# Kernel optimization log

Hardware: AMD Instinct MI355X
Metric: run time of the kernel (lower is better)

Reference implementation:

```python
import jax, jax.numpy as jnp
import numpy as np

V = 196608      # HEALPix nside=128 vertices
DEG = 9         # nnz per row (8 neighbors + self)
C = 64          # in_channels == out_channels
K = 8           # Chebyshev kernel_size
B = 1
EPS = 1e-5


def setup_inputs() -> dict:
    key = jax.random.key(0)
    ks = jax.random.split(key, 8)
    nnz = V * DEG
    x = jax.random.normal(ks[0], (B, V, C), dtype=jnp.float32)
    lap_rows = jnp.repeat(jnp.arange(V, dtype=jnp.int64), DEG)
    lap_cols = jax.random.randint(ks[1], (nnz,), 0, V, dtype=jnp.int64)
    lap_vals = jax.random.normal(ks[2], (nnz,), dtype=jnp.float32) * 0.1
    gamma = jnp.ones((C,), dtype=jnp.float32)
    beta = jnp.zeros((C,), dtype=jnp.float32)
    # Chebyshev weight [K, Fin, Fout], kaiming-like scale
    weight = jax.random.normal(ks[3], (K, C, C), dtype=jnp.float32) * (1.0 / np.sqrt(C * K))
    bias = jnp.zeros((C,), dtype=jnp.float32)
    return {"x": x, "lap_rows": lap_rows, "lap_cols": lap_cols, "lap_vals": lap_vals,
            "gamma": gamma, "beta": beta, "weight": weight, "bias": bias}


def _mish(h):
    return h * jnp.tanh(jax.nn.softplus(h))


def reference(x, lap_rows, lap_cols, lap_vals, gamma, beta, weight, bias):
    Bb, Vv, Cc = x.shape
    Kk = weight.shape[0]
    # BatchNorm1d (training-mode batch stats) over (B, V) per channel
    mean = jnp.mean(x, axis=(0, 1))
    var = jnp.var(x, axis=(0, 1))
    h = (x - mean) * jax.lax.rsqrt(var + EPS) * gamma + beta
    # Mish activation
    h = _mish(h)
    # Chebyshev spectral conv: x_k = 2*L@x_{k-1} - x_{k-2}
    def lap_mm(y):  # y: [V, M] sparse L @ y via gather + segment-sum scatter
        return jax.ops.segment_sum(lap_vals[:, None] * y[lap_cols], lap_rows,
                                   num_segments=Vv)
    x0 = jnp.transpose(h, (1, 0, 2)).reshape(Vv, Bb * Cc)  # [V, B*Fin]
    xs = [x0]
    if Kk > 1:
        xs.append(lap_mm(x0))
    for _ in range(2, Kk):
        xs.append(2.0 * lap_mm(xs[-1]) - xs[-2])
    Xk = jnp.stack(xs, axis=0).reshape(Kk, Vv, Bb, Cc)  # [K, V, B, Fin]
    out = jnp.einsum('kvbi,kio->bvo', Xk, weight) + bias  # [B, V, Fout]
    return out
```

## Files before the change

### kernel.cpp

```cpp
#include <hip/hip_runtime.h>
#include <math.h>

#define NV 196608
#define NDEG 9
#define NC 64
#define NK 8
#define TILE 64
#define NBLK (NV / TILE)
#define LDA 72
static constexpr float EPS = 1e-5f;

typedef __attribute__((ext_vector_type(8))) short bf16x8;
typedef __attribute__((ext_vector_type(4))) short bf16x4;
typedef __attribute__((ext_vector_type(4))) float f32x4;

__device__ __forceinline__ short f2bf(float f) {
    unsigned u = __float_as_uint(f);
    unsigned r = (u + 0x7fffu + ((u >> 16) & 1u)) >> 16;
    return (short)r;
}
__device__ __forceinline__ float bf2f(short h) {
    return __uint_as_float(((unsigned)(unsigned short)h) << 16);
}

__device__ __forceinline__ float mish_f(float h) {
    float t = __expf(fminf(h, 20.f));
    float p = 1.f + t;
    float p2 = p * p;
    return h * ((p2 - 1.f) / (p2 + 1.f));
}

__global__ void __launch_bounds__(256) stats_kernel(const float* __restrict__ x,
                                                    float* __restrict__ stats) {
    const float4* x4 = (const float4*)x;
    int t = blockIdx.x * 256 + threadIdx.x;
    int stride = gridDim.x * 256;
    float4 s = {0.f, 0.f, 0.f, 0.f}, ss = {0.f, 0.f, 0.f, 0.f};
    for (int i = t; i < NV * (NC / 4); i += stride) {
        float4 v = x4[i];
        s.x += v.x; s.y += v.y; s.z += v.z; s.w += v.w;
        ss.x += v.x * v.x; ss.y += v.y * v.y; ss.z += v.z * v.z; ss.w += v.w * v.w;
    }
    __shared__ float4 ls[256], lss[256];
    ls[threadIdx.x] = s;
    lss[threadIdx.x] = ss;
    __syncthreads();
    if (threadIdx.x < 64) {
        int ch = threadIdx.x;
        int g = ch >> 2, comp = ch & 3;
        float a = 0.f, b = 0.f;
        #pragma unroll
        for (int k = 0; k < 16; ++k) {
            float4 v1 = ls[k * 16 + g];
            float4 v2 = lss[k * 16 + g];
            a += (comp == 0) ? v1.x : (comp == 1) ? v1.y : (comp == 2) ? v1.z : v1.w;
            b += (comp == 0) ? v2.x : (comp == 1) ? v2.y : (comp == 2) ? v2.z : v2.w;
        }
        atomicAdd(&stats[ch], a);
        atomicAdd(&stats[64 + ch], b);
    }
}

__global__ void __launch_bounds__(256) wconv_kernel(const float* __restrict__ w,
                                                    unsigned short* __restrict__ Wb) {
    int idx = blockIdx.x * 256 + threadIdx.x;
    int i = idx & 63, o = (idx >> 6) & 63, k = idx >> 12;
    Wb[idx] = (unsigned short)f2bf(w[k * 4096 + i * 64 + o]);
}

__global__ void __launch_bounds__(256) bn_mish_k0(
    const float* __restrict__ x, const float* __restrict__ stats,
    const float* __restrict__ gamma, const float* __restrict__ beta,
    unsigned short* __restrict__ dst) {
    int lane = threadIdx.x & 63;
    int wave = threadIdx.x >> 6;
    int c4 = lane & 15, rg = lane >> 4;
    int tile0 = blockIdx.x * TILE;

    float4 sc, sh;
    {
        float4 su = ((const float4*)stats)[c4];
        float4 sq = ((const float4*)stats)[16 + c4];
        float4 g4 = ((const float4*)gamma)[c4];
        float4 b4 = ((const float4*)beta)[c4];
        #define BNC(comp) { float mu = su.comp * (1.f / NV);                     \
                            float va = sq.comp * (1.f / NV) - mu * mu;           \
                            float rs = rsqrtf(va + EPS);                         \
                            sc.comp = g4.comp * rs;                              \
                            sh.comp = b4.comp - mu * sc.comp; }
        BNC(x) BNC(y) BNC(z) BNC(w)
        #undef BNC
    }

    const float4* x4 = (const float4*)x;
    #pragma unroll
    for (int it = 0; it < 4; ++it) {
        int v = tile0 + wave * 16 + it * 4 + rg;
        float4 h = x4[v * 16 + c4];
        float4 m;
        m.x = mish_f(h.x * sc.x + sh.x);
        m.y = mish_f(h.y * sc.y + sh.y);
        m.z = mish_f(h.z * sc.z + sh.z);
        m.w = mish_f(h.w * sc.w + sh.w);
        bf16x4 xb = { f2bf(m.x), f2bf(m.y), f2bf(m.z), f2bf(m.w) };
        *(bf16x4*)(dst + (size_t)v * NC + 4 * c4) = xb;
    }
}

template <bool FIRST>
__global__ void __launch_bounds__(256) cheb_step(
    const int* __restrict__ cols, const float* __restrict__ vals,
    const unsigned short* __restrict__ src, const unsigned short* __restrict__ prev,
    unsigned short* __restrict__ dst) {
    int lane = threadIdx.x & 63;
    int wave = threadIdx.x >> 6;
    int c8 = lane & 7, rg = lane >> 3;
    int tile0 = blockIdx.x * TILE;

    #pragma unroll
    for (int it = 0; it < 2; ++it) {
        int v = tile0 + wave * 16 + it * 8 + rg;
        const int* cp = cols + v * NDEG;
        const float* vp = vals + v * NDEG;
        float s[8] = {0.f, 0.f, 0.f, 0.f, 0.f, 0.f, 0.f, 0.f};
        #pragma unroll
        for (int j = 0; j < NDEG; ++j) {
            int cj = cp[j];
            float aj = vp[j];
            bf16x8 g = *(const bf16x8*)(src + (size_t)cj * NC + c8 * 8);
            #pragma unroll
            for (int q = 0; q < 8; ++q) s[q] += aj * bf2f(g[q]);
        }
        bf16x8 xb;
        if (FIRST) {
            #pragma unroll
            for (int q = 0; q < 8; ++q) xb[q] = f2bf(s[q]);
        } else {
            bf16x8 p = *(const bf16x8*)(prev + (size_t)v * NC + c8 * 8);
            #pragma unroll
            for (int q = 0; q < 8; ++q) xb[q] = f2bf(2.f * s[q] - bf2f(p[q]));
        }
        *(bf16x8*)(dst + (size_t)v * NC + c8 * 8) = xb;
    }
}

__global__ void __launch_bounds__(256) gemm_bases(
    const unsigned short* __restrict__ basis, const unsigned short* __restrict__ Wb,
    const float* __restrict__ bias, float* __restrict__ out,
    int kb, int kc, int S, int first) {
    __shared__ short At[TILE * LDA];
    __shared__ short Wt[NC * LDA];
    int tid = threadIdx.x;
    int lane = tid & 63, wave = tid >> 6;
    int m16 = lane & 15, qq = lane >> 4;
    int tile0 = blockIdx.x * TILE;

    f32x4 acc[4];
    #pragma unroll
    for (int nt = 0; nt < 4; ++nt) acc[nt] = (f32x4){0.f, 0.f, 0.f, 0.f};

    #pragma unroll 1
    for (int j = 0; j < kc; ++j) {
        int k = kb + j;
        const unsigned short* bs = basis + (size_t)(k % S) * NV * NC + (size_t)tile0 * NC;
        const unsigned short* wsrc = Wb + (size_t)k * NC * NC;
        __syncthreads();
        #pragma unroll
        for (int h = 0; h < 2; ++h) {
            int ci = tid + h * 256;
            int r = ci >> 3, c = ci & 7;
            *(bf16x8*)&At[r * LDA + c * 8] = *(const bf16x8*)(bs + ci * 8);
            *(bf16x8*)&Wt[r * LDA + c * 8] = *(const bf16x8*)(wsrc + ci * 8);
        }
        __syncthreads();
        bf16x8 a0 = *(const bf16x8*)&At[(wave * 16 + m16) * LDA + qq * 8];
        bf16x8 a1 = *(const bf16x8*)&At[(wave * 16 + m16) * LDA + 32 + qq * 8];
        #pragma unroll
        for (int nt = 0; nt < 4; ++nt) {
            bf16x8 b0 = *(const bf16x8*)&Wt[(nt * 16 + m16) * LDA + qq * 8];
            bf16x8 b1 = *(const bf16x8*)&Wt[(nt * 16 + m16) * LDA + 32 + qq * 8];
            acc[nt] = __builtin_amdgcn_mfma_f32_16x16x32_bf16(a0, b0, acc[nt], 0, 0, 0);
            acc[nt] = __builtin_amdgcn_mfma_f32_16x16x32_bf16(a1, b1, acc[nt], 0, 0, 0);
        }
    }

    #pragma unroll
    for (int nt = 0; nt < 4; ++nt) {
        float bcol = bias[nt * 16 + m16];
        #pragma unroll
        for (int r = 0; r < 4; ++r) {
            int vout = tile0 + wave * 16 + qq * 4 + r;
            float* po = out + (size_t)vout * NC + nt * 16 + m16;
            *po = first ? (acc[nt][r] + bcol) : (*po + acc[nt][r]);
        }
    }
}

extern "C" void kernel_launch(void* const* d_in, const int* in_sizes, int n_in,
                              void* d_out, int out_size, void* d_ws, size_t ws_size,
                              hipStream_t stream) {
    const float* x      = (const float*)d_in[0];
    const int*   cols   = (const int*)  d_in[2];
    const float* vals   = (const float*)d_in[3];
    const float* gamma  = (const float*)d_in[4];
    const float* beta   = (const float*)d_in[5];
    const float* weight = (const float*)d_in[6];
    const float* bias   = (const float*)d_in[7];
    float* out = (float*)d_out;

    char* wsb = (char*)d_ws;
    float*          stats = (float*)wsb;
    unsigned short* Wb    = (unsigned short*)(wsb + 1024);
    unsigned short* basis = (unsigned short*)(wsb + 131072);
    const size_t SLOT = (size_t)NV * NC;

    int S = (int)((ws_size - 131072) / (SLOT * sizeof(unsigned short)));
    if (S > NK) S = NK;
    if (S < 3) S = 3;

    hipMemsetAsync(stats, 0, 1024, stream);
    wconv_kernel<<<128, 256, 0, stream>>>(weight, Wb);
    stats_kernel<<<1024, 256, 0, stream>>>(x, stats);
    bn_mish_k0<<<NBLK, 256, 0, stream>>>(x, stats, gamma, beta, basis);

    int kb = 0, gsize = S, first = 1;
    while (kb < NK) {
        int kc = (gsize < NK - kb) ? gsize : (NK - kb);
        for (int k = (kb == 0 ? 1 : kb); k < kb + kc; ++k) {
            const unsigned short* src = basis + (size_t)((k - 1) % S) * SLOT;
            unsigned short*       dst = basis + (size_t)(k % S) * SLOT;
            if (k == 1) {
                cheb_step<true><<<NBLK, 256, 0, stream>>>(cols, vals, src, src, dst);
            } else {
                const unsigned short* prev = basis + (size_t)((k - 2) % S) * SLOT;
                cheb_step<false><<<NBLK, 256, 0, stream>>>(cols, vals, src, prev, dst);
            }
        }
        gemm_bases<<<NBLK, 256, 0, stream>>>(basis, Wb, bias, out, kb, kc, S, first);
        first = 0;
        kb += kc;
        gsize = S - 2;
    }
}
```

Before: 458.0 us.

## Merge stats/weight kernels, batch gathers, drop LDS staging in GEMM, split GEMM

Folds the weight bf16 conversion into the stats kernel as extra blocks, so one launch is saved. In cheb_step, the column indices and values are now loaded as vectors, all nine neighbour gathers are issued before accumulating, and the prev/dst accesses use nontemporal hints. gemm_bases now reads A and W fragments straight from global memory instead of staging them through LDS with barriers. When the workspace holds all eight bases, the first GEMM runs over k=0..3 right after basis 3 is built, and a second GEMM covers k=4..7. The risks are more registers from the batched gathers and uncoalesced, repeated W reads without LDS.

Result: slower. 557.8 us (+21.8%).

```diff
diff --git a/kernel.cpp b/kernel.cpp
--- a/kernel.cpp
+++ b/kernel.cpp
@@ -7,12 +7,14 @@
 #define NK 8
 #define TILE 64
 #define NBLK (NV / TILE)
-#define LDA 72
+#define SLOT ((size_t)NV * NC)
 static constexpr float EPS = 1e-5f;
 
 typedef __attribute__((ext_vector_type(8))) short bf16x8;
 typedef __attribute__((ext_vector_type(4))) short bf16x4;
 typedef __attribute__((ext_vector_type(4))) float f32x4;
+typedef int   i32x4u __attribute__((ext_vector_type(4), aligned(4)));
+typedef float f32x4u __attribute__((ext_vector_type(4), aligned(4)));
 
 __device__ __forceinline__ short f2bf(float f) {
     unsigned u = __float_as_uint(f);
@@ -30,11 +32,18 @@
     return h * ((p2 - 1.f) / (p2 + 1.f));
 }
 
-__global__ void __launch_bounds__(256) stats_kernel(const float* __restrict__ x,
-                                                    float* __restrict__ stats) {
+__global__ void __launch_bounds__(256) stats_wconv_kernel(
+    const float* __restrict__ x, float* __restrict__ stats,
+    const float* __restrict__ w, unsigned short* __restrict__ Wb) {
+    if (blockIdx.x >= 1024) {
+        int idx = (blockIdx.x - 1024) * 256 + threadIdx.x;
+        int i = idx & 63, o = (idx >> 6) & 63, k = idx >> 12;
+        Wb[idx] = (unsigned short)f2bf(w[k * 4096 + i * 64 + o]);
+        return;
+    }
     const float4* x4 = (const float4*)x;
     int t = blockIdx.x * 256 + threadIdx.x;
-    int stride = gridDim.x * 256;
+    int stride = 1024 * 256;
     float4 s = {0.f, 0.f, 0.f, 0.f}, ss = {0.f, 0.f, 0.f, 0.f};
     for (int i = t; i < NV * (NC / 4); i += stride) {
         float4 v = x4[i];
@@ -59,13 +68,6 @@
         atomicAdd(&stats[ch], a);
         atomicAdd(&stats[64 + ch], b);
     }
-}
-
-__global__ void __launch_bounds__(256) wconv_kernel(const float* __restrict__ w,
-                                                    unsigned short* __restrict__ Wb) {
-    int idx = blockIdx.x * 256 + threadIdx.x;
-    int i = idx & 63, o = (idx >> 6) & 63, k = idx >> 12;
-    Wb[idx] = (unsigned short)f2bf(w[k * 4096 + i * 64 + o]);
 }
 
 __global__ void __launch_bounds__(256) bn_mish_k0(
@@ -122,25 +124,40 @@
         int v = tile0 + wave * 16 + it * 8 + rg;
         const int* cp = cols + v * NDEG;
         const float* vp = vals + v * NDEG;
+        i32x4u c03 = __builtin_nontemporal_load((const i32x4u*)cp);
+        i32x4u c47 = __builtin_nontemporal_load((const i32x4u*)(cp + 4));
+        int    cl8 = __builtin_nontemporal_load(cp + 8);
+        f32x4u a03 = __builtin_nontemporal_load((const f32x4u*)vp);
+        f32x4u a47 = __builtin_nontemporal_load((const f32x4u*)(vp + 4));
+        float  al8 = __builtin_nontemporal_load(vp + 8);
+
+        int   cj[NDEG] = { c03[0], c03[1], c03[2], c03[3],
+                           c47[0], c47[1], c47[2], c47[3], cl8 };
+        float aj[NDEG] = { a03[0], a03[1], a03[2], a03[3],
+                           a47[0], a47[1], a47[2], a47[3], al8 };
+
+        bf16x8 g[NDEG];
+        #pragma unroll
+        for (int j = 0; j < NDEG; ++j)
+            g[j] = *(const bf16x8*)(src + (size_t)cj[j] * NC + c8 * 8);
+
         float s[8] = {0.f, 0.f, 0.f, 0.f, 0.f, 0.f, 0.f, 0.f};
         #pragma unroll
-        for (int j = 0; j < NDEG; ++j) {
-            int cj = cp[j];
-            float aj = vp[j];
-            bf16x8 g = *(const bf16x8*)(src + (size_t)cj * NC + c8 * 8);
+        for (int j = 0; j < NDEG; ++j)
             #pragma unroll
-            for (int q = 0; q < 8; ++q) s[q] += aj * bf2f(g[q]);
-        }
+            for (int q = 0; q < 8; ++q) s[q] += aj[j] * bf2f(g[j][q]);
+
         bf16x8 xb;
         if (FIRST) {
             #pragma unroll
             for (int q = 0; q < 8; ++q) xb[q] = f2bf(s[q]);
         } else {
-            bf16x8 p = *(const bf16x8*)(prev + (size_t)v * NC + c8 * 8);
+            bf16x8 p = __builtin_nontemporal_load(
+                           (const bf16x8*)(prev + (size_t)v * NC + c8 * 8));
             #pragma unroll
             for (int q = 0; q < 8; ++q) xb[q] = f2bf(2.f * s[q] - bf2f(p[q]));
         }
-        *(bf16x8*)(dst + (size_t)v * NC + c8 * 8) = xb;
+        __builtin_nontemporal_store(xb, (bf16x8*)(dst + (size_t)v * NC + c8 * 8));
     }
 }
 
@@ -148,10 +165,8 @@
     const unsigned short* __restrict__ basis, const unsigned short* __restrict__ Wb,
     const float* __restrict__ bias, float* __restrict__ out,
     int kb, int kc, int S, int first) {
-    __shared__ short At[TILE * LDA];
-    __shared__ short Wt[NC * LDA];
-    int tid = threadIdx.x;
-    int lane = tid & 63, wave = tid >> 6;
+    int lane = threadIdx.x & 63;
+    int wave = threadIdx.x >> 6;
     int m16 = lane & 15, qq = lane >> 4;
     int tile0 = blockIdx.x * TILE;
 
@@ -162,23 +177,16 @@
     #pragma unroll 1
     for (int j = 0; j < kc; ++j) {
         int k = kb + j;
-        const unsigned short* bs = basis + (size_t)(k % S) * NV * NC + (size_t)tile0 * NC;
-        const unsigned short* wsrc = Wb + (size_t)k * NC * NC;
-        __syncthreads();
-        #pragma unroll
-        for (int h = 0; h < 2; ++h) {
-            int ci = tid + h * 256;
-            int r = ci >> 3, c = ci & 7;
-            *(bf16x8*)&At[r * LDA + c * 8] = *(const bf16x8*)(bs + ci * 8);
-            *(bf16x8*)&Wt[r * LDA + c * 8] = *(const bf16x8*)(wsrc + ci * 8);
-        }
-        __syncthreads();
-        bf16x8 a0 = *(const bf16x8*)&At[(wave * 16 + m16) * LDA + qq * 8];
-        bf16x8 a1 = *(const bf16x8*)&At[(wave * 16 + m16) * LDA + 32 + qq * 8];
+        const unsigned short* bs =
+            basis + (size_t)(k % S) * SLOT + (size_t)(tile0 + wave * 16 + m16) * NC;
+        bf16x8 a0 = __builtin_nontemporal_load((const bf16x8*)(bs + qq * 8));
+        bf16x8 a1 = __builtin_nontemporal_load((const bf16x8*)(bs + 32 + qq * 8));
+        const unsigned short* wk = Wb + (size_t)k * NC * NC;
         #pragma unroll
         for (int nt = 0; nt < 4; ++nt) {
-            bf16x8 b0 = *(const bf16x8*)&Wt[(nt * 16 + m16) * LDA + qq * 8];
-            bf16x8 b1 = *(const bf16x8*)&Wt[(nt * 16 + m16) * LDA + 32 + qq * 8];
+            const unsigned short* wr = wk + (nt * 16 + m16) * NC;
+            bf16x8 b0 = *(const bf16x8*)(wr + qq * 8);
+            bf16x8 b1 = *(const bf16x8*)(wr + 32 + qq * 8);
             acc[nt] = __builtin_amdgcn_mfma_f32_16x16x32_bf16(a0, b0, acc[nt], 0, 0, 0);
             acc[nt] = __builtin_amdgcn_mfma_f32_16x16x32_bf16(a1, b1, acc[nt], 0, 0, 0);
         }
@@ -212,33 +220,47 @@
     float*          stats = (float*)wsb;
     unsigned short* Wb    = (unsigned short*)(wsb + 1024);
     unsigned short* basis = (unsigned short*)(wsb + 131072);
-    const size_t SLOT = (size_t)NV * NC;
 
     int S = (int)((ws_size - 131072) / (SLOT * sizeof(unsigned short)));
     if (S > NK) S = NK;
     if (S < 3) S = 3;
 
     hipMemsetAsync(stats, 0, 1024, stream);
-    wconv_kernel<<<128, 256, 0, stream>>>(weight, Wb);
-    stats_kernel<<<1024, 256, 0, stream>>>(x, stats);
+    stats_wconv_kernel<<<1152, 256, 0, stream>>>(x, stats, weight, Wb);
     bn_mish_k0<<<NBLK, 256, 0, stream>>>(x, stats, gamma, beta, basis);
 
-    int kb = 0, gsize = S, first = 1;
-    while (kb < NK) {
-        int kc = (gsize < NK - kb) ? gsize : (NK - kb);
-        for (int k = (kb == 0 ? 1 : kb); k < kb + kc; ++k) {
-            const unsigned short* src = basis + (size_t)((k - 1) % S) * SLOT;
-            unsigned short*       dst = basis + (size_t)(k % S) * SLOT;
+    if (S >= NK) {
+        for (int k = 1; k < NK; ++k) {
+            const unsigned short* src = basis + (size_t)(k - 1) * SLOT;
+            unsigned short*       dst = basis + (size_t)k * SLOT;
             if (k == 1) {
                 cheb_step<true><<<NBLK, 256, 0, stream>>>(cols, vals, src, src, dst);
             } else {
-                const unsigned short* prev = basis + (size_t)((k - 2) % S) * SLOT;
+                const unsigned short* prev = basis + (size_t)(k - 2) * SLOT;
                 cheb_step<false><<<NBLK, 256, 0, stream>>>(cols, vals, src, prev, dst);
             }
-        }
-        gemm_bases<<<NBLK, 256, 0, stream>>>(basis, Wb, bias, out, kb, kc, S, first);
-        first = 0;
-        kb += kc;
-        gsize = S - 2;
-    }
-}
+            if (k == 3)
+                gemm_bases<<<NBLK, 256, 0, stream>>>(basis, Wb, bias, out, 0, 4, NK, 1);
+        }
+        gemm_bases<<<NBLK, 256, 0, stream>>>(basis, Wb, bias, out, 4, 4, NK, 0);
+    } else {
+        int kb = 0, gsize = S, first = 1;
+        while (kb < NK) {
+            int kc = (gsize < NK - kb) ? gsize : (NK - kb);
+            for (int k = (kb == 0 ? 1 : kb); k < kb + kc; ++k) {
+                const unsigned short* src = basis + (size_t)((k - 1) % S) * SLOT;
+                unsigned short*       dst = basis + (size_t)(k % S) * SLOT;
+                if (k == 1) {
+                    cheb_step<true><<<NBLK, 256, 0, stream>>>(cols, vals, src, src, dst);
+                } else {
+                    const unsigned short* prev = basis + (size_t)((k - 2) % S) * SLOT;
+                    cheb_step<false><<<NBLK, 256, 0, stream>>>(cols, vals, src, prev, dst);
+                }
+            }
+            gemm_bases<<<NBLK, 256, 0, stream>>>(basis, Wb, bias, out, kb, kc, S, first);
+            first = 0;
+            kb += kc;
+            gsize = S - 2;
+        }
+    }
+}
```
